# Kernel tuning notes

Measured on AMD Instinct MI355X. Metric: run time of the kernel, lower is better.

## Reference

```python
import jax, jax.numpy as jnp
import numpy as np

M, IN_F, OUT_F = 16384, 2048, 2048

def sign_fn(x):
    # torch.sign(torch.sign(x) + 0.5): maps 0 -> +1, otherwise +/-1
    return jnp.sign(jnp.sign(x) + 0.5)

def setup_inputs() -> dict:
    key = jax.random.key(0)
    kx, kw = jax.random.split(key)
    # Upstream BNN activations are binary +/-1 (required for the packed-bit
    # backward in the original module to be exact).
    x = sign_fn(jax.random.normal(kx, (M, IN_F), dtype=jnp.float32))
    weight = jax.random.uniform(kw, (OUT_F, IN_F), dtype=jnp.float32) * 0.01
    return {"x": x, "weight": weight}

def reference(x, weight):
    # xnor=False path: SignFunctionNoSTE -> binarize weight, then dense matmul
    b_weight = sign_fn(weight)          # [OUT_F, IN_F], values in {-1, +1}
    return x @ b_weight.T               # [M, OUT_F]
```

## Files before the change

### kernel.cpp

```cpp
#include <hip/hip_runtime.h>
#include <stdint.h>

typedef unsigned long long u64;

#define M_DIM 16384
#define N_DIM 2048
#define K_DIM 2048


#define BM 256
#define BN 256
#define BK 128
#define NST (K_DIM / BK)

typedef int   v4i  __attribute__((ext_vector_type(4)));
typedef int   v8i  __attribute__((ext_vector_type(8)));
typedef float v16f __attribute__((ext_vector_type(16)));

__device__ __forceinline__ void gld16(void* lds_base, const void* gsrc) {
    __builtin_amdgcn_global_load_lds(
        (const __attribute__((address_space(1))) uint32_t*)gsrc,
        (__attribute__((address_space(3))) uint32_t*)lds_base,
        16, 0, 0);
}

__device__ __forceinline__ int pkn(float4 a, float4 b) {
    int r;
    r  = (a.x < 0.0f ? 0xA : 0x2);
    r |= (a.y < 0.0f ? 0xA : 0x2) << 4;
    r |= (a.z < 0.0f ? 0xA : 0x2) << 8;
    r |= (a.w < 0.0f ? 0xA : 0x2) << 12;
    r |= (b.x < 0.0f ? 0xA : 0x2) << 16;
    r |= (b.y < 0.0f ? 0xA : 0x2) << 20;
    r |= (b.z < 0.0f ? 0xA : 0x2) << 24;
    r |= (b.w < 0.0f ? 0xA : 0x2) << 28;
    return r;
}

__global__ __launch_bounds__(256) void pack_fp4_kernel(
        const float* __restrict__ src, char* __restrict__ dst) {
    const int wid  = (blockIdx.x * 256 + threadIdx.x) >> 6;
    const int lane = threadIdx.x & 63;
    const int t    = wid & 7;
    const int sub  = (wid >> 3) & 1;
    const int st   = (wid >> 4) & 15;
    const int blk  = wid >> 8;
    const int row  = blk * 256 + t * 32 + (lane & 31);
    const int kb   = st * 128 + sub * 64 + (lane >> 5) * 32;
    const float4* p = (const float4*)(src + (size_t)row * K_DIM + kb);
    int4 o;
    o.x = pkn(p[0], p[1]);
    o.y = pkn(p[2], p[3]);
    o.z = pkn(p[4], p[5]);
    o.w = pkn(p[6], p[7]);
    *(int4*)(dst + (size_t)wid * 1024 + lane * 16) = o;
}

__device__ __forceinline__ v8i up8(v4i v) {
    v8i r;
    r[0] = v[0]; r[1] = v[1]; r[2] = v[2]; r[3] = v[3];
    r[4] = 0;    r[5] = 0;    r[6] = 0;    r[7] = 0;
    return r;
}

__global__ __launch_bounds__(512, 2) void bgemm_fp4_kernel(
        const char* __restrict__ Ap, const char* __restrict__ Bp,
        float* __restrict__ C) {
    __shared__ __align__(16) char lds[2][32 * 1024];

    const int t    = threadIdx.x;
    const int lane = t & 63;
    const int wv   = t >> 6;
    const int wm   = (wv >> 1) & 3;
    const int wn   = wv & 1;

    const int id    = blockIdx.x;
    const int xcd   = id & 7;
    const int idx   = id >> 3;
    const int m_blk = xcd * 8 + (idx & 7);
    const int n_blk = idx >> 3;

    const char* aG = Ap + (size_t)m_blk * (NST * 16384);
    const char* bG = Bp + (size_t)n_blk * (NST * 16384);

    v16f acc[2][4];
#pragma unroll
    for (int i = 0; i < 2; ++i)
#pragma unroll
        for (int j = 0; j < 4; ++j)
#pragma unroll
            for (int q = 0; q < 16; ++q) acc[i][j][q] = 0.0f;

    auto dma = [&](int s, int buf) {
        const char* a = aG + (size_t)s * 16384;
        const char* b = bG + (size_t)s * 16384;
#pragma unroll
        for (int r = 0; r < 4; ++r) {
            const int reg = wv * 4 + r;
            const char* g = (reg < 16) ? (a + reg * 1024)
                                       : (b + (reg - 16) * 1024);
            gld16(&lds[buf][reg * 1024], g + lane * 16);
        }
    };

    auto compute = [&](int buf) {
        const char* As = lds[buf];
        const char* Bs = lds[buf] + 16384;
#pragma unroll
        for (int sub = 0; sub < 2; ++sub) {
            v8i af[2], bf[4];
#pragma unroll
            for (int i = 0; i < 2; ++i)
                af[i] = up8(*(const v4i*)(As + (sub * 8 + wm * 2 + i) * 1024 + lane * 16));
#pragma unroll
            for (int j = 0; j < 4; ++j)
                bf[j] = up8(*(const v4i*)(Bs + (sub * 8 + wn * 4 + j) * 1024 + lane * 16));
#pragma unroll
            for (int i = 0; i < 2; ++i)
#pragma unroll
                for (int j = 0; j < 4; ++j)
                    acc[i][j] = __builtin_amdgcn_mfma_scale_f32_32x32x64_f8f6f4(
                        af[i], bf[j], acc[i][j],
                        4, 4,
                        0, 0x7F7F7F7F,
                        0, 0x7F7F7F7F);
        }
    };

    dma(0, 0);
    __syncthreads();
#pragma unroll 1
    for (int s = 0; s < NST; ++s) {
        if (s + 1 < NST) dma(s + 1, (s + 1) & 1);
        compute(s & 1);
        __syncthreads();
    }

    const int col = lane & 31;
    const int rq  = (lane >> 5) * 4;
#pragma unroll
    for (int i = 0; i < 2; ++i) {
#pragma unroll
        for (int j = 0; j < 4; ++j) {
            const int mbase = m_blk * BM + (wm * 2 + i) * 32;
            const int nbase = n_blk * BN + (wn * 4 + j) * 32;
#pragma unroll
            for (int q = 0; q < 16; ++q) {
                const int row = mbase + (q & 3) + 8 * (q >> 2) + rq;
                C[(size_t)row * N_DIM + nbase + col] = acc[i][j][q];
            }
        }
    }
}

#define KC 32
#define KT 16
struct alignas(16) u64x2 { u64 x, y; };

__global__ __launch_bounds__(256) void pack_sign_kernel(
        const float* __restrict__ in, u64* __restrict__ out, int ngroups) {
    int wid  = (blockIdx.x * 256 + threadIdx.x) >> 6;
    int lane = threadIdx.x & 63;
    if (wid >= ngroups) return;
    const float4* p = reinterpret_cast<const float4*>(in) + (size_t)wid * 64 + lane;
    float4 v = *p;
    u64 b0 = __ballot(v.x < 0.0f);
    u64 b1 = __ballot(v.y < 0.0f);
    u64 b2 = __ballot(v.z < 0.0f);
    u64 b3 = __ballot(v.w < 0.0f);
    if (lane == 0) {
        u64* o = out + (size_t)wid * 4;
        o[0] = b0; o[1] = b1; o[2] = b2; o[3] = b3;
    }
}

__global__ __launch_bounds__(256, 2) void bgemm_kernel(
        const u64* __restrict__ A, const u64* __restrict__ B,
        float* __restrict__ C) {
    __shared__ u64 As[KT][128];
    __shared__ u64 Bs[KT][128];
    const int t     = threadIdx.x;
    const int m_blk = blockIdx.y << 7;
    const int n_blk = blockIdx.x << 7;
    const int lane = t & 63;
    const int wave = t >> 6;
    const int tm   = lane >> 3;
    const int tn   = lane & 7;
    const int m0   = ((wave >> 1) << 6) + (tm << 3);
    const int n0   = ((wave & 1) << 6) + (tn << 3);
    unsigned acc[8][8];
#pragma unroll
    for (int i = 0; i < 8; ++i)
#pragma unroll
        for (int j = 0; j < 8; ++j) acc[i][j] = 0u;
    const int sr = t >> 3;
    const int sc = (t << 1) & 15;
    for (int ks = 0; ks < K_DIM / (KT * 64); ++ks) {
        const int cbase = ks * KT;
#pragma unroll
        for (int i = 0; i < 4; ++i) {
            int r = i * 32 + sr;
            u64x2 va = *reinterpret_cast<const u64x2*>(A + (size_t)(m_blk + r) * KC + cbase + sc);
            As[sc][r] = va.x; As[sc + 1][r] = va.y;
            u64x2 vb = *reinterpret_cast<const u64x2*>(B + (size_t)(n_blk + r) * KC + cbase + sc);
            Bs[sc][r] = vb.x; Bs[sc + 1][r] = vb.y;
        }
        __syncthreads();
#pragma unroll 1
        for (int c = 0; c < KT; ++c) {
            u64 a[8], b[8];
#pragma unroll
            for (int i = 0; i < 4; ++i) {
                u64x2 va = *reinterpret_cast<const u64x2*>(&As[c][m0 + 2 * i]);
                a[2 * i] = va.x; a[2 * i + 1] = va.y;
                u64x2 vb = *reinterpret_cast<const u64x2*>(&Bs[c][n0 + 2 * i]);
                b[2 * i] = vb.x; b[2 * i + 1] = vb.y;
            }
#pragma unroll
            for (int i = 0; i < 8; ++i)
#pragma unroll
                for (int j = 0; j < 8; ++j)
                    acc[i][j] += (unsigned)__builtin_popcountll(a[i] ^ b[j]);
        }
        __syncthreads();
    }
#pragma unroll
    for (int i = 0; i < 8; ++i) {
        float* o = C + (size_t)(m_blk + m0 + i) * N_DIM + n_blk + n0;
        float4 v0, v1;
        v0.x = (float)(K_DIM - 2 * (int)acc[i][0]);
        v0.y = (float)(K_DIM - 2 * (int)acc[i][1]);
        v0.z = (float)(K_DIM - 2 * (int)acc[i][2]);
        v0.w = (float)(K_DIM - 2 * (int)acc[i][3]);
        v1.x = (float)(K_DIM - 2 * (int)acc[i][4]);
        v1.y = (float)(K_DIM - 2 * (int)acc[i][5]);
        v1.z = (float)(K_DIM - 2 * (int)acc[i][6]);
        v1.w = (float)(K_DIM - 2 * (int)acc[i][7]);
        *reinterpret_cast<float4*>(o)     = v0;
        *reinterpret_cast<float4*>(o + 4) = v1;
    }
}

extern "C" void kernel_launch(void* const* d_in, const int* in_sizes, int n_in,
                              void* d_out, int out_size, void* d_ws, size_t ws_size,
                              hipStream_t stream) {
    const float* x = (const float*)d_in[0];
    const float* w = (const float*)d_in[1];
    float* out = (float*)d_out;

    const size_t needA = (size_t)M_DIM * K_DIM / 2;
    const size_t needB = (size_t)N_DIM * K_DIM / 2;
    if (ws_size >= needA + needB) {
        char* Ap = (char*)d_ws;
        char* Bp = Ap + needA;
        pack_fp4_kernel<<<4096, 256, 0, stream>>>(x, Ap);
        pack_fp4_kernel<<<512, 256, 0, stream>>>(w, Bp);
        bgemm_fp4_kernel<<<(M_DIM / BM) * (N_DIM / BN), 512, 0, stream>>>(Ap, Bp, out);
    } else {
        u64* xb = (u64*)d_ws;
        u64* wb = xb + (size_t)M_DIM * KC;
        int xgroups = (M_DIM * K_DIM) / 256;
        int wgroups = (N_DIM * K_DIM) / 256;
        pack_sign_kernel<<<xgroups / 4, 256, 0, stream>>>(x, xb, xgroups);
        pack_sign_kernel<<<wgroups / 4, 256, 0, stream>>>(w, wb, wgroups);
        bgemm_kernel<<<dim3(N_DIM / 128, M_DIM / 128), 256, 0, stream>>>(xb, wb, out);
    }
}
```

Measured before the change: 286.3 us.

## Load A fragments directly to registers, stage only B in LDS, fuse pack kernels

The GEMM now loads the packed activation (A) fragments straight from global memory into registers, prefetched one stage ahead with explicit ping-pong register buffers. Only the weight tile is staged in LDS, which halves LDS use per block. The two packing launches are merged into one kernel, and the output stores become nontemporal. The aim is to cut LDS traffic and footprint and one launch, at the cost of more registers and direct global loads with less coalescing reuse.

New measurement: 288.8 us. No clear change (+0.9%).

```diff
diff --git a/kernel.cpp b/kernel.cpp
--- a/kernel.cpp
+++ b/kernel.cpp
@@ -37,9 +37,14 @@
     return r;
 }
 
-__global__ __launch_bounds__(256) void pack_fp4_kernel(
-        const float* __restrict__ src, char* __restrict__ dst) {
-    const int wid  = (blockIdx.x * 256 + threadIdx.x) >> 6;
+__global__ __launch_bounds__(256) void pack_fp4_all_kernel(
+        const float* __restrict__ x, const float* __restrict__ w,
+        char* __restrict__ Ap, char* __restrict__ Bp) {
+    const int bid  = blockIdx.x;
+    const bool isA = bid < 4096;
+    const float* src = isA ? x : w;
+    char*        dst = isA ? Ap : Bp;
+    const int wid  = (isA ? bid : bid - 4096) * 4 + ((threadIdx.x >> 6) & 3);
     const int lane = threadIdx.x & 63;
     const int t    = wid & 7;
     const int sub  = (wid >> 3) & 1;
@@ -66,7 +71,7 @@
 __global__ __launch_bounds__(512, 2) void bgemm_fp4_kernel(
         const char* __restrict__ Ap, const char* __restrict__ Bp,
         float* __restrict__ C) {
-    __shared__ __align__(16) char lds[2][32 * 1024];
+    __shared__ __align__(16) char lds[2][16 * 1024];
 
     const int t    = threadIdx.x;
     const int lane = t & 63;
@@ -80,7 +85,7 @@
     const int m_blk = xcd * 8 + (idx & 7);
     const int n_blk = idx >> 3;
 
-    const char* aG = Ap + (size_t)m_blk * (NST * 16384);
+    const char* aG = Ap + (size_t)m_blk * (NST * 16384) + lane * 16;
     const char* bG = Bp + (size_t)n_blk * (NST * 16384);
 
     v16f acc[2][4];
@@ -92,47 +97,51 @@
             for (int q = 0; q < 16; ++q) acc[i][j][q] = 0.0f;
 
     auto dma = [&](int s, int buf) {
+        const char* b = bG + (size_t)s * 16384;
+#pragma unroll
+        for (int r = 0; r < 2; ++r) {
+            const int reg = wv * 2 + r;
+            gld16(&lds[buf][reg * 1024], b + reg * 1024 + lane * 16);
+        }
+    };
+    auto afload = [&](int s, v4i af[2][2]) {
         const char* a = aG + (size_t)s * 16384;
-        const char* b = bG + (size_t)s * 16384;
-#pragma unroll
-        for (int r = 0; r < 4; ++r) {
-            const int reg = wv * 4 + r;
-            const char* g = (reg < 16) ? (a + reg * 1024)
-                                       : (b + (reg - 16) * 1024);
-            gld16(&lds[buf][reg * 1024], g + lane * 16);
-        }
+#pragma unroll
+        for (int sub = 0; sub < 2; ++sub)
+#pragma unroll
+            for (int i = 0; i < 2; ++i)
+                af[sub][i] = *(const v4i*)(a + (sub * 8 + wm * 2 + i) * 1024);
     };
-
-    auto compute = [&](int buf) {
-        const char* As = lds[buf];
-        const char* Bs = lds[buf] + 16384;
+    auto compute = [&](int buf, v4i af[2][2]) {
+        const char* Bs = lds[buf];
 #pragma unroll
         for (int sub = 0; sub < 2; ++sub) {
-            v8i af[2], bf[4];
-#pragma unroll
-            for (int i = 0; i < 2; ++i)
-                af[i] = up8(*(const v4i*)(As + (sub * 8 + wm * 2 + i) * 1024 + lane * 16));
+            v4i bf[4];
 #pragma unroll
             for (int j = 0; j < 4; ++j)
-                bf[j] = up8(*(const v4i*)(Bs + (sub * 8 + wn * 4 + j) * 1024 + lane * 16));
+                bf[j] = *(const v4i*)(Bs + (sub * 8 + wn * 4 + j) * 1024 + lane * 16);
 #pragma unroll
             for (int i = 0; i < 2; ++i)
 #pragma unroll
                 for (int j = 0; j < 4; ++j)
                     acc[i][j] = __builtin_amdgcn_mfma_scale_f32_32x32x64_f8f6f4(
-                        af[i], bf[j], acc[i][j],
+                        up8(af[sub][i]), up8(bf[j]), acc[i][j],
                         4, 4,
                         0, 0x7F7F7F7F,
                         0, 0x7F7F7F7F);
         }
     };
 
-    dma(0, 0);
+    v4i af0[2][2], af1[2][2];
+    dma(0, 0); afload(0, af0);
     __syncthreads();
 #pragma unroll 1
-    for (int s = 0; s < NST; ++s) {
-        if (s + 1 < NST) dma(s + 1, (s + 1) & 1);
-        compute(s & 1);
+    for (int s = 0; s < NST; s += 2) {
+        dma(s + 1, 1); afload(s + 1, af1);
+        compute(0, af0);
+        __syncthreads();
+        if (s + 2 < NST) { dma(s + 2, 0); afload(s + 2, af0); }
+        compute(1, af1);
         __syncthreads();
     }
 
@@ -147,7 +156,8 @@
 #pragma unroll
             for (int q = 0; q < 16; ++q) {
                 const int row = mbase + (q & 3) + 8 * (q >> 2) + rq;
-                C[(size_t)row * N_DIM + nbase + col] = acc[i][j][q];
+                __builtin_nontemporal_store(
+                    acc[i][j][q], &C[(size_t)row * N_DIM + nbase + col]);
             }
         }
     }
@@ -253,8 +263,7 @@
     if (ws_size >= needA + needB) {
         char* Ap = (char*)d_ws;
         char* Bp = Ap + needA;
-        pack_fp4_kernel<<<4096, 256, 0, stream>>>(x, Ap);
-        pack_fp4_kernel<<<512, 256, 0, stream>>>(w, Bp);
+        pack_fp4_all_kernel<<<4608, 256, 0, stream>>>(x, w, Ap, Bp);
         bgemm_fp4_kernel<<<(M_DIM / BM) * (N_DIM / BN), 512, 0, stream>>>(Ap, Bp, out);
     } else {
         u64* xb = (u64*)d_ws;
```
